# Performance work log

Measured on AMD Instinct MI355X. Metric: run time of the kernel, lower is better.

Reference implementation:

```python
import jax, jax.numpy as jnp
import numpy as np

IMG = 224
PATCH_SIZE = 2      # stride of the output patch grid (output_size = H // PATCH_SIZE)
PATCH_PIXEL = 4     # samples per patch side (deformable resampling resolution)
EMBED = 192
OFFSET_EMBED = 2    # (dx, dy) per patch
IN_CH = 3
BATCH = 32


def setup_inputs() -> dict:
    key = jax.random.key(0)
    k1, k2, k3 = jax.random.split(key, 3)
    x = jax.random.normal(k1, (BATCH, IN_CH, IMG, IMG), jnp.float32)
    conv_w = jax.random.normal(k2, (EMBED, IN_CH, 3, 3), jnp.float32) * 0.05
    conv_b = jnp.zeros((EMBED,), jnp.float32)
    off_w = jax.random.normal(k3, (OFFSET_EMBED, EMBED), jnp.float32) * 0.02
    return {"x": x, "conv_w": conv_w, "conv_b": conv_b, "off_w": off_w}


def _bilinear_gather(img, ys, xs):
    # img: [B, C, H, W]; ys, xs: [B, P] float pixel coords. Border-clamped bilinear.
    B, C, H, W = img.shape
    y0 = jnp.floor(ys)
    x0 = jnp.floor(xs)
    wy = (ys - y0)[:, None, :]
    wx = (xs - x0)[:, None, :]
    y0i = jnp.clip(y0.astype(jnp.int32), 0, H - 1)
    y1i = jnp.clip(y0i + 1, 0, H - 1)
    x0i = jnp.clip(x0.astype(jnp.int32), 0, W - 1)
    x1i = jnp.clip(x0i + 1, 0, W - 1)
    flat = img.reshape(B, C, H * W)
    P = ys.shape[1]

    def g(yi, xi):
        idx = (yi * W + xi)[:, None, :]  # [B,1,P]
        return jnp.take_along_axis(flat, jnp.broadcast_to(idx, (B, C, P)), axis=2)

    v00 = g(y0i, x0i)
    v01 = g(y0i, x1i)
    v10 = g(y1i, x0i)
    v11 = g(y1i, x1i)
    return (v00 * (1 - wy) * (1 - wx) + v01 * (1 - wy) * wx
            + v10 * wy * (1 - wx) + v11 * wy * wx)  # [B,C,P]


def reference(x, conv_w, conv_b, off_w):
    B, C, H, W = x.shape
    # PatchEmbed: conv k3 s2 p1 -> flatten -> tokens [B, N, E]
    feat = jax.lax.conv_general_dilated(
        x, conv_w, window_strides=(2, 2), padding=((1, 1), (1, 1)),
        dimension_numbers=('NCHW', 'OIHW', 'NCHW')) + conv_b[None, :, None, None]
    Hf, Wf = feat.shape[2], feat.shape[3]
    tokens = feat.reshape(B, EMBED, Hf * Wf).transpose(0, 2, 1)  # [B,N,E]
    # offset predictor: GELU (exact) then bias-free linear
    pred = jax.nn.gelu(tokens, approximate=False) @ off_w.T      # [B,N,2]

    Ho, Wo = H // PATCH_SIZE, W // PATCH_SIZE  # == (Hf, Wf) by construction
    off = pred.reshape(B, Ho, Wo, OFFSET_EMBED) * PATCH_SIZE     # pixel-space offsets

    # Deformable patch resampling: each output patch samples a PATCH_PIXEL^2 grid
    # centered at its shifted patch center.
    cy = (jnp.arange(Ho, dtype=jnp.float32) + 0.5) * PATCH_SIZE
    cx = (jnp.arange(Wo, dtype=jnp.float32) + 0.5) * PATCH_SIZE
    local = ((jnp.arange(PATCH_PIXEL, dtype=jnp.float32) + 0.5) / PATCH_PIXEL
             * PATCH_SIZE - PATCH_SIZE / 2)
    ys = (cy[None, :, None, None, None] + off[..., 1][:, :, :, None, None]
          + local[None, None, None, :, None])
    xs = (cx[None, None, :, None, None] + off[..., 0][:, :, :, None, None]
          + local[None, None, None, None, :])
    shape5 = (B, Ho, Wo, PATCH_PIXEL, PATCH_PIXEL)
    ys = jnp.broadcast_to(ys, shape5).reshape(B, -1)
    xs = jnp.broadcast_to(xs, shape5).reshape(B, -1)

    sampled = _bilinear_gather(x, ys, xs)  # [B,C,Ho*Wo*pp*pp]
    out = sampled.reshape(B, C, Ho, Wo, PATCH_PIXEL, PATCH_PIXEL)
    out = out.transpose(0, 1, 2, 4, 3, 5).reshape(
        B, C, Ho * PATCH_PIXEL, Wo * PATCH_PIXEL)
    return out
```

## Files before the change

kernel.cpp:

```cpp
#include <hip/hip_runtime.h>
#include <hip/hip_bf16.h>

#define IMG   224
#define HO    112
#define WO_   112
#define EMBED 192
#define BATCH 32
#define NPOS  (BATCH * HO * WO_)
#define TPW   4

typedef __attribute__((ext_vector_type(8))) short short8;
typedef __attribute__((ext_vector_type(4))) float float4v;

__device__ __forceinline__ short f2bf(float f) {
    unsigned u = __builtin_bit_cast(unsigned, f);
    u += 0x7FFFu + ((u >> 16) & 1u);
    return (short)(u >> 16);
}

__device__ __forceinline__ float fast_gelu(float a) {
    float e = __builtin_amdgcn_exp2f(a * -2.45546507f);
    return a * __builtin_amdgcn_rcpf(1.0f + e);
}

__device__ __forceinline__ short8 gather_afrag(const float* __restrict__ x,
                                               int pos, int quad) {
    int wo = pos % WO_;
    int t2 = pos / WO_;
    int ho = t2 % HO;
    int b  = t2 / HO;
    int iy0 = 2 * ho - 1, ix0 = 2 * wo - 1;
    const float* xb = x + (size_t)b * 3 * IMG * IMG;
    short8 a;
#pragma unroll
    for (int j = 0; j < 8; ++j) {
        int k = quad * 8 + j;
        float v;
        if (k < 27) {
            int c  = k / 9;
            int r9 = k % 9;
            int iy = iy0 + r9 / 3;
            int ix = ix0 + r9 % 3;
            v = (iy >= 0 && iy < IMG && ix >= 0 && ix < IMG)
                    ? xb[(size_t)c * IMG * IMG + iy * IMG + ix] : 0.0f;
        } else {
            v = (k == 27) ? 1.0f : 0.0f;
        }
        a[j] = f2bf(v);
    }
    return a;
}

__global__ __launch_bounds__(256)
void fused_kernel(const float* __restrict__ x,
                  const float* __restrict__ conv_w,
                  const float* __restrict__ conv_b,
                  const float* __restrict__ off_w,
                  float* __restrict__ out) {
    __shared__ float s_off[4][TPW][16][2];

    int lane = threadIdx.x & 63;
    int wv   = threadIdx.x >> 6;
    int gw   = blockIdx.x * 4 + wv;
    int base = gw * (16 * TPW);
    int col  = lane & 15;
    int quad = lane >> 4;

    short8 bfrag[12];
#pragma unroll
    for (int nt = 0; nt < 12; ++nt) {
        int ch = nt * 16 + col;
#pragma unroll
        for (int j = 0; j < 8; ++j) {
            int k = quad * 8 + j;
            float v = (k < 27) ? conv_w[ch * 27 + k]
                               : ((k == 27) ? conv_b[ch] : 0.0f);
            bfrag[nt][j] = f2bf(v);
        }
    }
    float owx[12], owy[12];
#pragma unroll
    for (int nt = 0; nt < 12; ++nt) {
        owx[nt] = off_w[nt * 16 + col] * 2.0f;
        owy[nt] = off_w[EMBED + nt * 16 + col] * 2.0f;
    }

    short8 afrag = gather_afrag(x, base + col, quad);
    for (int it = 0; it < TPW; ++it) {
        short8 nxt;
        if (it + 1 < TPW) nxt = gather_afrag(x, base + (it + 1) * 16 + col, quad);

        float ox[4] = {0, 0, 0, 0}, oy[4] = {0, 0, 0, 0};
#pragma unroll
        for (int nt = 0; nt < 12; ++nt) {
            float4v c = {0.0f, 0.0f, 0.0f, 0.0f};
            c = __builtin_amdgcn_mfma_f32_16x16x32_bf16(afrag, bfrag[nt], c, 0, 0, 0);
#pragma unroll
            for (int r = 0; r < 4; ++r) {
                float g = fast_gelu(c[r]);
                ox[r] = fmaf(g, owx[nt], ox[r]);
                oy[r] = fmaf(g, owy[nt], oy[r]);
            }
        }
#pragma unroll
        for (int d = 1; d < 16; d <<= 1) {
#pragma unroll
            for (int r = 0; r < 4; ++r) {
                ox[r] += __shfl_xor(ox[r], d, 64);
                oy[r] += __shfl_xor(oy[r], d, 64);
            }
        }
        if (col == 0) {
#pragma unroll
            for (int r = 0; r < 4; ++r) {
                s_off[wv][it][quad * 4 + r][0] = ox[r];
                s_off[wv][it][quad * 4 + r][1] = oy[r];
            }
        }
        afrag = nxt;
    }
    __syncthreads();

    int patch_local = lane >> 2;
    int px = lane & 3;
    for (int it = 0; it < TPW; ++it) {
        int pos = base + it * 16 + patch_local;
        int wo = pos % WO_;
        int t2 = pos / WO_;
        int ho = t2 % HO;
        int b  = t2 / HO;

        float ofx = s_off[wv][it][patch_local][0];
        float ofy = s_off[wv][it][patch_local][1];

        float xs = (wo + 0.5f) * 2.0f + ofx + ((px + 0.5f) * 0.5f - 1.0f);
        float x0f = floorf(xs);
        float wx = xs - x0f;
        int x0 = (int)x0f; x0 = min(max(x0, 0), IMG - 1);
        int x1 = min(x0 + 1, IMG - 1);
        float wx1 = 1.0f - wx;

        const float* xb = x + (size_t)b * 3 * IMG * IMG;
        size_t obase = ((size_t)b * 3) * 448 * 448;
        int ox_ = wo * 4 + px;

#pragma unroll
        for (int py = 0; py < 4; ++py) {
            float ys = (ho + 0.5f) * 2.0f + ofy + ((py + 0.5f) * 0.5f - 1.0f);
            float y0f = floorf(ys);
            float wy = ys - y0f;
            int y0 = (int)y0f; y0 = min(max(y0, 0), IMG - 1);
            int y1 = min(y0 + 1, IMG - 1);
            float wy1 = 1.0f - wy;
            int oy_ = ho * 4 + py;

#pragma unroll
            for (int c = 0; c < 3; ++c) {
                const float* xc = xb + (size_t)c * IMG * IMG;
                const float* row0 = xc + y0 * IMG;
                const float* row1 = xc + y1 * IMG;
                float v00 = row0[x0], v01 = row0[x1];
                float v10 = row1[x0], v11 = row1[x1];
                float top = v00 * wx1 + v01 * wx;
                float bot = v10 * wx1 + v11 * wx;
                out[obase + ((size_t)c * 448 + oy_) * 448 + ox_] =
                    top * wy1 + bot * wy;
            }
        }
    }
}

extern "C" void kernel_launch(void* const* d_in, const int* in_sizes, int n_in,
                              void* d_out, int out_size, void* d_ws, size_t ws_size,
                              hipStream_t stream) {
    const float* x      = (const float*)d_in[0];
    const float* conv_w = (const float*)d_in[1];
    const float* conv_b = (const float*)d_in[2];
    const float* off_w  = (const float*)d_in[3];
    float* out = (float*)d_out;

    fused_kernel<<<NPOS / 256, 256, 0, stream>>>(x, conv_w, conv_b, off_w, out);
}
```

Before: 150.8 us.

## Drop shared-memory offset staging and precompute im2col offsets per block row

Each wave now resamples right after computing its 16 offsets, selecting the offset from registers instead of going through LDS and a block barrier. Blocks are shrunk to 128 threads and aligned to one image, so the batch index is per block. Im2col addresses come from precomputed per-lane offsets with a fast path for interior rows. The bilinear path uses paired adjacent loads with select-based clamping and FMA interpolation. This removes the gather prefetch overlap, which may expose load latency.

```diff
diff --git a/kernel.cpp b/kernel.cpp
--- a/kernel.cpp
+++ b/kernel.cpp
@@ -1,12 +1,14 @@
 #include <hip/hip_runtime.h>
-#include <hip/hip_bf16.h>
 
 #define IMG   224
+#define IMG2  (IMG * IMG)
 #define HO    112
 #define WO_   112
 #define EMBED 192
 #define BATCH 32
 #define NPOS  (BATCH * HO * WO_)
+#define PPB   (HO * WO_)
+#define BLK_POS 128
 #define TPW   4
 
 typedef __attribute__((ext_vector_type(8))) short short8;
@@ -23,48 +25,34 @@
     return a * __builtin_amdgcn_rcpf(1.0f + e);
 }
 
-__device__ __forceinline__ short8 gather_afrag(const float* __restrict__ x,
-                                               int pos, int quad) {
-    int wo = pos % WO_;
-    int t2 = pos / WO_;
-    int ho = t2 % HO;
-    int b  = t2 / HO;
-    int iy0 = 2 * ho - 1, ix0 = 2 * wo - 1;
-    const float* xb = x + (size_t)b * 3 * IMG * IMG;
-    short8 a;
-#pragma unroll
-    for (int j = 0; j < 8; ++j) {
-        int k = quad * 8 + j;
-        float v;
-        if (k < 27) {
-            int c  = k / 9;
-            int r9 = k % 9;
-            int iy = iy0 + r9 / 3;
-            int ix = ix0 + r9 % 3;
-            v = (iy >= 0 && iy < IMG && ix >= 0 && ix < IMG)
-                    ? xb[(size_t)c * IMG * IMG + iy * IMG + ix] : 0.0f;
-        } else {
-            v = (k == 27) ? 1.0f : 0.0f;
-        }
-        a[j] = f2bf(v);
-    }
-    return a;
-}
-
-__global__ __launch_bounds__(256)
+__global__ __launch_bounds__(128)
 void fused_kernel(const float* __restrict__ x,
                   const float* __restrict__ conv_w,
                   const float* __restrict__ conv_b,
                   const float* __restrict__ off_w,
                   float* __restrict__ out) {
-    __shared__ float s_off[4][TPW][16][2];
+    const int lane = threadIdx.x & 63;
+    const int wv   = threadIdx.x >> 6;
+    const int col  = lane & 15;
+    const int quad = lane >> 4;
 
-    int lane = threadIdx.x & 63;
-    int wv   = threadIdx.x >> 6;
-    int gw   = blockIdx.x * 4 + wv;
-    int base = gw * (16 * TPW);
-    int col  = lane & 15;
-    int quad = lane >> 4;
+    const int b   = blockIdx.x / (PPB / BLK_POS);
+    const int pb0 = (blockIdx.x % (PPB / BLK_POS)) * BLK_POS + wv * 64;
+    const float* __restrict__ xb = x + (size_t)b * 3 * IMG2;
+    float* __restrict__ ob = out + (size_t)b * 3 * (448 * 448);
+
+    int  off[8];
+    bool isr[8];
+    bool k27[8];
+#pragma unroll
+    for (int j = 0; j < 8; ++j) {
+        int k = quad * 8 + j;
+        int c = k / 9, r9 = k % 9;
+        int dy = r9 / 3, dx = r9 % 3;
+        isr[j] = (k < 27);
+        k27[j] = (k == 27);
+        off[j] = isr[j] ? (c * IMG2 + dy * IMG + dx) : 0;
+    }
 
     short8 bfrag[12];
 #pragma unroll
@@ -85,16 +73,41 @@
         owy[nt] = off_w[EMBED + nt * 16 + col] * 2.0f;
     }
 
-    short8 afrag = gather_afrag(x, base + col, quad);
     for (int it = 0; it < TPW; ++it) {
-        short8 nxt;
-        if (it + 1 < TPW) nxt = gather_afrag(x, base + (it + 1) * 16 + col, quad);
+        int p   = pb0 + it * 16;
+        int ho  = p / WO_;
+        int wo0 = p % WO_;
+        int iy0 = 2 * ho - 1;
+        int ixl = 2 * (wo0 + col) - 1;
+        int base = iy0 * IMG + ixl;
+
+        short8 a;
+        if (ho > 0 && wo0 > 0) {
+#pragma unroll
+            for (int j = 0; j < 8; ++j) {
+                float v = isr[j] ? xb[base + off[j]] : 0.0f;
+                if (k27[j]) v = 1.0f;
+                a[j] = f2bf(v);
+            }
+        } else {
+#pragma unroll
+            for (int j = 0; j < 8; ++j) {
+                int k = quad * 8 + j;
+                int r9 = k % 9;
+                int dy = r9 / 3, dx = r9 % 3;
+                bool ok = isr[j] && (iy0 + dy >= 0) && (ixl + dx >= 0);
+                int ad = ok ? (base + off[j]) : 0;
+                float v = ok ? xb[ad] : 0.0f;
+                if (k27[j]) v = 1.0f;
+                a[j] = f2bf(v);
+            }
+        }
 
         float ox[4] = {0, 0, 0, 0}, oy[4] = {0, 0, 0, 0};
 #pragma unroll
         for (int nt = 0; nt < 12; ++nt) {
             float4v c = {0.0f, 0.0f, 0.0f, 0.0f};
-            c = __builtin_amdgcn_mfma_f32_16x16x32_bf16(afrag, bfrag[nt], c, 0, 0, 0);
+            c = __builtin_amdgcn_mfma_f32_16x16x32_bf16(a, bfrag[nt], c, 0, 0, 0);
 #pragma unroll
             for (int r = 0; r < 4; ++r) {
                 float g = fast_gelu(c[r]);
@@ -110,61 +123,47 @@
                 oy[r] += __shfl_xor(oy[r], d, 64);
             }
         }
-        if (col == 0) {
-#pragma unroll
-            for (int r = 0; r < 4; ++r) {
-                s_off[wv][it][quad * 4 + r][0] = ox[r];
-                s_off[wv][it][quad * 4 + r][1] = oy[r];
-            }
-        }
-        afrag = nxt;
-    }
-    __syncthreads();
 
-    int patch_local = lane >> 2;
-    int px = lane & 3;
-    for (int it = 0; it < TPW; ++it) {
-        int pos = base + it * 16 + patch_local;
-        int wo = pos % WO_;
-        int t2 = pos / WO_;
-        int ho = t2 % HO;
-        int b  = t2 / HO;
+        int patch = lane >> 2;
+        int rsel  = patch & 3;
+        int px    = lane & 3;
+        float s01x = (rsel & 1) ? ox[1] : ox[0];
+        float s23x = (rsel & 1) ? ox[3] : ox[2];
+        float ofx  = (rsel & 2) ? s23x : s01x;
+        float s01y = (rsel & 1) ? oy[1] : oy[0];
+        float s23y = (rsel & 1) ? oy[3] : oy[2];
+        float ofy  = (rsel & 2) ? s23y : s01y;
 
-        float ofx = s_off[wv][it][patch_local][0];
-        float ofy = s_off[wv][it][patch_local][1];
-
-        float xs = (wo + 0.5f) * 2.0f + ofx + ((px + 0.5f) * 0.5f - 1.0f);
+        int wo = wo0 + patch;
+        float xs = 2.0f * wo + 0.25f + 0.5f * px + ofx;
         float x0f = floorf(xs);
-        float wx = xs - x0f;
+        float wx  = xs - x0f;
         int x0 = (int)x0f; x0 = min(max(x0, 0), IMG - 1);
-        int x1 = min(x0 + 1, IMG - 1);
-        float wx1 = 1.0f - wx;
-
-        const float* xb = x + (size_t)b * 3 * IMG * IMG;
-        size_t obase = ((size_t)b * 3) * 448 * 448;
-        int ox_ = wo * 4 + px;
+        int xq = min(x0, IMG - 2);
+        bool selx = (x0 > xq);
+        int ocol = wo * 4 + px;
 
 #pragma unroll
         for (int py = 0; py < 4; ++py) {
-            float ys = (ho + 0.5f) * 2.0f + ofy + ((py + 0.5f) * 0.5f - 1.0f);
+            float ys = 2.0f * ho + 0.25f + 0.5f * py + ofy;
             float y0f = floorf(ys);
-            float wy = ys - y0f;
+            float wy  = ys - y0f;
             int y0 = (int)y0f; y0 = min(max(y0, 0), IMG - 1);
-            int y1 = min(y0 + 1, IMG - 1);
-            float wy1 = 1.0f - wy;
-            int oy_ = ho * 4 + py;
+            int dyo = (y0 < IMG - 1) ? IMG : 0;
+            int rb = y0 * IMG + xq;
+            int orow = (ho * 4 + py) * 448 + ocol;
 
 #pragma unroll
             for (int c = 0; c < 3; ++c) {
-                const float* xc = xb + (size_t)c * IMG * IMG;
-                const float* row0 = xc + y0 * IMG;
-                const float* row1 = xc + y1 * IMG;
-                float v00 = row0[x0], v01 = row0[x1];
-                float v10 = row1[x0], v11 = row1[x1];
-                float top = v00 * wx1 + v01 * wx;
-                float bot = v10 * wx1 + v11 * wx;
-                out[obase + ((size_t)c * 448 + oy_) * 448 + ox_] =
-                    top * wy1 + bot * wy;
+                int v0 = rb + c * IMG2;
+                int v1 = v0 + dyo;
+                float A0 = xb[v0], A1 = xb[v0 + 1];
+                float B0 = xb[v1], B1 = xb[v1 + 1];
+                float v00 = selx ? A1 : A0;
+                float v10 = selx ? B1 : B0;
+                float top = fmaf(wx, A1 - v00, v00);
+                float bot = fmaf(wx, B1 - v10, v10);
+                ob[c * 200704 + orow] = fmaf(wy, bot - top, top);
             }
         }
     }
@@ -179,5 +178,5 @@
     const float* off_w  = (const float*)d_in[3];
     float* out = (float*)d_out;
 
-    fused_kernel<<<NPOS / 256, 256, 0, stream>>>(x, conv_w, conv_b, off_w, out);
+    fused_kernel<<<NPOS / BLK_POS, 128, 0, stream>>>(x, conv_w, conv_b, off_w, out);
 }
```

New measurement: 153.5 us. No clear change (+1.8%).
